# Performance work log

Hardware: AMD Instinct MI355X
Metric: run time of the kernel (lower is better)

Reference implementation:

```python
import jax, jax.numpy as jnp
import numpy as np

N = 100000
E = 3200000
IN_DIM = 512
HID = 256
NUM_CLASSES = 16
P_DROP = 0.5
EPS_BN = 1e-5


def setup_inputs() -> dict:
    key = jax.random.key(0)
    ks = jax.random.split(key, 6)
    x = jax.random.normal(ks[0], (N, IN_DIM), jnp.float32)
    edge_src = jax.random.randint(ks[1], (E,), 0, N, dtype=jnp.int32)
    edge_dst = jax.random.randint(ks[2], (E,), 0, N, dtype=jnp.int32)
    # Glorot-ish init for GraphConv weights (bias=False in the module)
    W1 = jax.random.normal(ks[3], (IN_DIM, HID), jnp.float32) / np.sqrt(IN_DIM).astype(np.float32)
    W2 = jax.random.normal(ks[4], (HID, NUM_CLASSES), jnp.float32) / np.sqrt(HID).astype(np.float32)
    W3 = jax.random.normal(ks[5], (HID, NUM_CLASSES), jnp.float32) / np.sqrt(HID).astype(np.float32)
    return {"x": x, "W1": W1, "W2": W2, "W3": W3,
            "edge_src": edge_src, "edge_dst": edge_dst}


def _graph_conv(h, W, edge_src, edge_dst, out_inv_sqrt, in_inv_sqrt):
    # DGL GraphConv, norm='both', bias=False:
    #   rst = D_in^{-1/2} * A_agg( D_out^{-1/2} * h @ W )
    # Apply W before aggregation (out_dim <= in_dim here); same math as DGL.
    h = h * out_inv_sqrt[:, None]          # [N, d_in]
    h = h @ W                              # [N, d_out]
    agg = jax.ops.segment_sum(h[edge_src], edge_dst, num_segments=h.shape[0])
    return agg * in_inv_sqrt[:, None]


def _dropout(key, x, p=P_DROP):
    keep = jax.random.bernoulli(key, 1.0 - p, x.shape)
    return jnp.where(keep, x / (1.0 - p), jnp.zeros((), x.dtype))


def reference(x, W1, W2, W3, edge_src, edge_dst):
    n = x.shape[0]
    ones = jnp.ones(edge_src.shape[0], x.dtype)
    out_deg = jax.ops.segment_sum(ones, edge_src, num_segments=n)
    in_deg = jax.ops.segment_sum(ones, edge_dst, num_segments=n)
    out_is = jnp.maximum(out_deg, 1.0) ** -0.5   # DGL clamps degree to min 1
    in_is = jnp.maximum(in_deg, 1.0) ** -0.5

    k1, k2a, k2b, keps = jax.random.split(jax.random.key(42), 4)

    # gc1 + relu
    h = _dropout(k1, x)
    h = jax.nn.relu(_graph_conv(h, W1, edge_src, edge_dst, out_is, in_is))

    # BatchNorm1d(affine=False, track_running_stats=False): batch stats
    mean = jnp.mean(h, axis=0)
    var = jnp.var(h, axis=0)
    h = (h - mean) * jax.lax.rsqrt(var + EPS_BN)

    # gc2 (mu) and gc3 (logvar), each with its own dropout of hidden1
    mu = _graph_conv(_dropout(k2a, h), W2, edge_src, edge_dst, out_is, in_is)
    logvar = _graph_conv(_dropout(k2b, h), W3, edge_src, edge_dst, out_is, in_is)

    # reparameterize (training): eps * exp(logvar) + mu  (note: exp(logvar), per source)
    eps = jax.random.normal(keps, mu.shape, mu.dtype)
    return eps * jnp.exp(logvar) + mu
```

## Files before the change

### kernel.cpp

```cpp
#include <hip/hip_runtime.h>
#include <stdint.h>

#define N_NODES 100000
#define N_EDGES 3200000
#define IN_DIM  512
#define HID     256
#define NCLS    16

#define DBLK   256
#define DCHUNK (N_EDGES / DBLK)
#define DWIN2  50000
#define NBKT   98
#define NTILE  ((N_NODES + 255) / 256)

typedef unsigned short u16;
typedef __attribute__((ext_vector_type(8))) short short8;
typedef __attribute__((ext_vector_type(4))) float float4v;

__device__ __forceinline__ float bf2f(u16 u) {
  return __uint_as_float(((uint32_t)u) << 16);
}
__device__ __forceinline__ u16 f2bf(float f) {
  uint32_t u = __float_as_uint(f);
  return (u16)((u + 0x7fffu + ((u >> 16) & 1u)) >> 16);
}
__device__ __forceinline__ void acc8(float* a, uint4 v) {
  a[0] += bf2f((u16)(v.x & 0xffffu)); a[1] += bf2f((u16)(v.x >> 16));
  a[2] += bf2f((u16)(v.y & 0xffffu)); a[3] += bf2f((u16)(v.y >> 16));
  a[4] += bf2f((u16)(v.z & 0xffffu)); a[5] += bf2f((u16)(v.z >> 16));
  a[6] += bf2f((u16)(v.w & 0xffffu)); a[7] += bf2f((u16)(v.w >> 16));
}

__device__ __forceinline__ void gload16(const void* g, void* l) {
  __builtin_amdgcn_global_load_lds(
      (const __attribute__((address_space(1))) uint32_t*)g,
      (__attribute__((address_space(3))) uint32_t*)l, 16, 0, 0);
}

__host__ __device__ __forceinline__ uint32_t rotl32(uint32_t v, int d) {
  return (v << d) | (v >> (32 - d));
}

__host__ __device__ __forceinline__ void threefry2x32(uint32_t k0, uint32_t k1,
    uint32_t x0, uint32_t x1, uint32_t& o0, uint32_t& o1) {
  uint32_t ks0 = k0, ks1 = k1, ks2 = k0 ^ k1 ^ 0x1BD11BDAu;
  x0 += ks0; x1 += ks1;
#define TF_R(r) { x0 += x1; x1 = rotl32(x1, r); x1 ^= x0; }
  TF_R(13) TF_R(15) TF_R(26) TF_R(6)
  x0 += ks1; x1 += ks2 + 1u;
  TF_R(17) TF_R(29) TF_R(16) TF_R(24)
  x0 += ks2; x1 += ks0 + 2u;
  TF_R(13) TF_R(15) TF_R(26) TF_R(6)
  x0 += ks0; x1 += ks1 + 3u;
  TF_R(17) TF_R(29) TF_R(16) TF_R(24)
  x0 += ks1; x1 += ks2 + 4u;
  TF_R(13) TF_R(15) TF_R(26) TF_R(6)
  x0 += ks2; x1 += ks0 + 5u;
#undef TF_R
  o0 = x0; o1 = x1;
}

__host__ __device__ __forceinline__ uint32_t tf_bits32(uint32_t k0, uint32_t k1, uint32_t idx) {
  uint32_t o0, o1;
  threefry2x32(k0, k1, 0u, idx, o0, o1);
  return o0 ^ o1;
}

__device__ __forceinline__ float erfinv_f32(float x) {
  float w = -log1pf(-x * x);
  float p;
  if (w < 5.0f) {
    w -= 2.5f;
    p = 2.81022636e-08f;
    p = fmaf(p, w, 3.43273939e-07f);
    p = fmaf(p, w, -3.5233877e-06f);
    p = fmaf(p, w, -4.39150654e-06f);
    p = fmaf(p, w, 0.00021858087f);
    p = fmaf(p, w, -0.00125372503f);
    p = fmaf(p, w, -0.00417768164f);
    p = fmaf(p, w, 0.246640727f);
    p = fmaf(p, w, 1.50140941f);
  } else {
    w = sqrtf(w) - 3.0f;
    p = -0.000200214257f;
    p = fmaf(p, w, 0.000100950558f);
    p = fmaf(p, w, 0.00134934322f);
    p = fmaf(p, w, -0.00367342844f);
    p = fmaf(p, w, 0.00573950773f);
    p = fmaf(p, w, -0.0076224613f);
    p = fmaf(p, w, 0.00943887047f);
    p = fmaf(p, w, 1.00167406f);
    p = fmaf(p, w, 2.83297682f);
  }
  return p * x;
}

__global__ __launch_bounds__(1024) void hist_k(
    const int* __restrict__ esrc, const int* __restrict__ edst,
    u16* __restrict__ P16, uint32_t* __restrict__ bofs_g) {
  __shared__ uint32_t h32[DWIN2 / 2];
  __shared__ uint32_t bcnt[NBKT + 1];
  const int b = blockIdx.x, tid = threadIdx.x;
  const int ebase = b * DCHUNK;
  if (tid < NBKT + 1) bcnt[tid] = 0u;
  for (int w = 0; w < 2; ++w) {
    const int lo = w * DWIN2;
    for (int i = tid; i < DWIN2 / 2; i += 1024) h32[i] = 0u;
    __syncthreads();
    for (int e = ebase + tid; e < ebase + DCHUNK; e += 1024) {
      int s = esrc[e], d = edst[e];
      unsigned su = (unsigned)(s - lo);
      if (su < (unsigned)DWIN2) atomicAdd(&h32[su >> 1], 1u << ((su & 1) * 16));
      unsigned du = (unsigned)(d - lo);
      if (du < (unsigned)DWIN2) atomicAdd(&h32[du >> 1], 0x100u << ((du & 1) * 16));
      if (w == 0) atomicAdd(&bcnt[d >> 10], 1u);
    }
    __syncthreads();
    for (int i = tid; i < DWIN2 / 2; i += 1024) {
      *(uint32_t*)(P16 + (size_t)b * N_NODES + lo + 2 * i) = h32[i];
    }
    __syncthreads();
  }
  if (tid == 0) {
    uint32_t run = 0;
    for (int k = 0; k < NBKT; ++k) { uint32_t c = bcnt[k]; bcnt[k] = run; run += c; }
    bcnt[NBKT] = run;
  }
  __syncthreads();
  if (tid < NBKT + 1) bofs_g[b * (NBKT + 1) + tid] = bcnt[tid];
}

__global__ void degsum_k(const u16* __restrict__ P16, float* __restrict__ out_is,
                         float* __restrict__ in_is, int* __restrict__ row_ofs,
                         int* __restrict__ tile_sum) {
  const int tid = threadIdx.x;
  const int n = blockIdx.x * 256 + tid;
  const int lane = tid & 63, wv = tid >> 6;
  uint32_t to = 0, ti = 0;
  if (n < N_NODES) {
#pragma unroll 8
    for (int b = 0; b < DBLK; ++b) {
      uint32_t v = P16[(size_t)b * N_NODES + n];
      to += v & 0xffu; ti += v >> 8;
    }
    out_is[n] = rsqrtf(fmaxf((float)to, 1.0f));
    in_is[n]  = rsqrtf(fmaxf((float)ti, 1.0f));
  }
  int sc = (int)ti;
#pragma unroll
  for (int d = 1; d < 64; d <<= 1) {
    int t = __shfl_up(sc, d, 64);
    if (lane >= d) sc += t;
  }
  __shared__ int ws[4];
  if (lane == 63) ws[wv] = sc;
  __syncthreads();
  int wbase = 0;
#pragma unroll
  for (int i = 0; i < 4; ++i) if (i < wv) wbase += ws[i];
  if (n < N_NODES) row_ofs[n] = wbase + sc - (int)ti;
  if (tid == 0) tile_sum[blockIdx.x] = ws[0] + ws[1] + ws[2] + ws[3];
}

__global__ void fixup_k(const int* __restrict__ tile_sum, int* __restrict__ row_ofs) {
  const int b = blockIdx.x, tid = threadIdx.x;
  const int lane = tid & 63, wv = tid >> 6;
  int v = 0;
  if (tid < b) v = tile_sum[tid];
  if (tid + 256 < b) v += tile_sum[tid + 256];
#pragma unroll
  for (int m = 1; m < 64; m <<= 1) v += __shfl_xor(v, m, 64);
  __shared__ int wr[4];
  if (lane == 0) wr[wv] = v;
  __syncthreads();
  const int base = wr[0] + wr[1] + wr[2] + wr[3];
  const int n = b * 256 + tid;
  if (n < N_NODES) row_ofs[n] += base;
  if (b == (int)gridDim.x - 1 && tid == 0) row_ofs[N_NODES] = base + tile_sum[b];
}

__global__ __launch_bounds__(1024) void partition_k(
    const int* __restrict__ esrc, const int* __restrict__ edst,
    const uint32_t* __restrict__ bofs_g, unsigned long long* __restrict__ ebuf) {
  __shared__ uint32_t bcur[NBKT];
  const int b = blockIdx.x, tid = threadIdx.x;
  if (tid < NBKT) bcur[tid] = bofs_g[b * (NBKT + 1) + tid];
  __syncthreads();
  const int ebase = b * DCHUNK;
  for (int e = ebase + tid; e < ebase + DCHUNK; e += 1024) {
    int d = edst[e], s = esrc[e];
    uint32_t slot = atomicAdd(&bcur[d >> 10], 1u);
    ebuf[(size_t)b * DCHUNK + slot] = ((unsigned long long)(uint32_t)s << 32) | (uint32_t)d;
  }
}

__global__ __launch_bounds__(1024) void bplace_k(
    const unsigned long long* __restrict__ ebuf, const uint32_t* __restrict__ bofs_g,
    const int* __restrict__ row_ofs, int* __restrict__ csr) {
  __shared__ uint32_t cur[1024];
  const int k = blockIdx.x, tid = threadIdx.x;
  const int lane = tid & 63, wv = tid >> 6;
  const int dbase = k << 10;
  int nd = N_NODES - dbase; if (nd > 1024) nd = 1024;
  if (tid < nd) cur[tid] = (uint32_t)row_ofs[dbase + tid];
  __syncthreads();
  for (int b = wv; b < DBLK; b += 16) {
    uint32_t st = bofs_g[b * (NBKT + 1) + k];
    uint32_t en = bofs_g[b * (NBKT + 1) + k + 1];
    for (uint32_t i = st + lane; i < en; i += 64) {
      unsigned long long v = ebuf[(size_t)b * DCHUNK + i];
      int d = (int)(uint32_t)(v & 0xffffffffu);
      int s = (int)(uint32_t)(v >> 32);
      uint32_t slot = atomicAdd(&cur[d - dbase], 1u);
      csr[slot] = s;
    }
  }
}

__global__ void cast_w_k(const float* __restrict__ W1, const float* __restrict__ W2,
                         const float* __restrict__ W3, u16* __restrict__ W1t,
                         u16* __restrict__ Wt23) {
  int idx = blockIdx.x * blockDim.x + threadIdx.x;
  if (idx < IN_DIM * HID) {
    int k = idx >> 8, n = idx & 255;
    W1t[n * IN_DIM + k] = f2bf(W1[idx]);
  } else {
    int t = idx - IN_DIM * HID;
    int n = t >> 8, k = t & 255;
    float v = (n < 16) ? W2[k * NCLS + n] : W3[k * NCLS + (n - 16)];
    Wt23[n * HID + k] = f2bf(v);
  }
}

#define G1_BM 128
#define G1_BKC 8
__global__ __launch_bounds__(512, 2) void gemm1_k(
    const float* __restrict__ x, const float* __restrict__ out_is,
    uint32_t k0, uint32_t k1,
    const u16* __restrict__ W1t, u16* __restrict__ X1b) {
  __shared__ u16 As[G1_BM * 64];
  __shared__ u16 Bs[256 * 64];
  const int tid = threadIdx.x;
  const int wid = tid >> 6, lane = tid & 63;
  const int wr = wid >> 2, wc = wid & 3;
  const int m16 = lane & 15, q = lane >> 4;
  const int srow = lane >> 3, schunk = lane & 7;
  const long base_row = (long)blockIdx.x * G1_BM;

  const int arow_l = tid >> 2, acp = tid & 3;
  const long agrow = base_row + arow_l;
  const long asrow = (agrow < N_NODES) ? agrow : (N_NODES - 1);
  const float asc = 2.0f * out_is[asrow];
  const float* xrow = x + asrow * IN_DIM;
  const int aw0 = ((2 * acp)     ^ (arow_l & 7)) * 8;
  const int aw1 = ((2 * acp + 1) ^ (arow_l & 7)) * 8;

  float4v acc[4][4];
#pragma unroll
  for (int i = 0; i < 4; ++i)
#pragma unroll
    for (int j = 0; j < 4; ++j) acc[i][j] = (float4v)0.0f;

  for (int ks = 0; ks < IN_DIM / 64; ++ks) {
    const int kbase = ks * 64 + acp * 16;
    float4 f0 = *(const float4*)(xrow + kbase);
    float4 f1 = *(const float4*)(xrow + kbase + 4);
    float4 f2 = *(const float4*)(xrow + kbase + 8);
    float4 f3 = *(const float4*)(xrow + kbase + 12);
    float xv[16] = {f0.x, f0.y, f0.z, f0.w, f1.x, f1.y, f1.z, f1.w,
                    f2.x, f2.y, f2.z, f2.w, f3.x, f3.y, f3.z, f3.w};
    const uint32_t ibase = (uint32_t)asrow * IN_DIM + (uint32_t)kbase;
    u16 ob[16];
#pragma unroll
    for (int j = 0; j < 16; ++j) {
      uint32_t bits = tf_bits32(k0, k1, ibase + (uint32_t)j);
      ob[j] = f2bf((bits >> 31) ? 0.0f : xv[j] * asc);
    }
    uint4 pka, pkb;
    pka.x = (uint32_t)ob[0] | ((uint32_t)ob[1] << 16);
    pka.y = (uint32_t)ob[2] | ((uint32_t)ob[3] << 16);
    pka.z = (uint32_t)ob[4] | ((uint32_t)ob[5] << 16);
    pka.w = (uint32_t)ob[6] | ((uint32_t)ob[7] << 16);
    pkb.x = (uint32_t)ob[8] | ((uint32_t)ob[9] << 16);
    pkb.y = (uint32_t)ob[10] | ((uint32_t)ob[11] << 16);
    pkb.z = (uint32_t)ob[12] | ((uint32_t)ob[13] << 16);
    pkb.w = (uint32_t)ob[14] | ((uint32_t)ob[15] << 16);
    *(uint4*)(As + arow_l * 64 + aw0) = pka;
    *(uint4*)(As + arow_l * 64 + aw1) = pkb;
#pragma unroll
    for (int i = 0; i < 4; ++i) {
      int j = wid * 4 + i;
      int n = j * 8 + srow;
      int gch = ks * G1_BKC + (schunk ^ (n & 7));
      gload16(W1t + (size_t)n * IN_DIM + gch * 8, Bs + j * 512);
    }
    __syncthreads();
#pragma unroll
    for (int kk = 0; kk < 2; ++kk) {
      short8 a[4], b[4];
      const int kq = kk * 4 + q;
      const int c = kq ^ (m16 & 7);
#pragma unroll
      for (int rt = 0; rt < 4; ++rt) {
        int row = wr * 64 + rt * 16 + m16;
        a[rt] = *(const short8*)(As + row * 64 + c * 8);
      }
#pragma unroll
      for (int ct = 0; ct < 4; ++ct) {
        int n = wc * 64 + ct * 16 + m16;
        b[ct] = *(const short8*)(Bs + n * 64 + c * 8);
      }
#pragma unroll
      for (int rt = 0; rt < 4; ++rt)
#pragma unroll
        for (int ct = 0; ct < 4; ++ct)
          acc[rt][ct] = __builtin_amdgcn_mfma_f32_16x16x32_bf16(a[rt], b[ct], acc[rt][ct], 0, 0, 0);
    }
    __syncthreads();
  }
#pragma unroll
  for (int rt = 0; rt < 4; ++rt) {
#pragma unroll
    for (int r = 0; r < 4; ++r) {
      long grow = base_row + wr * 64 + rt * 16 + q * 4 + r;
      if (grow < N_NODES) {
#pragma unroll
        for (int ct = 0; ct < 4; ++ct)
          X1b[grow * HID + wc * 64 + ct * 16 + m16] = f2bf(acc[rt][ct][r]);
      }
    }
  }
}

__global__ __launch_bounds__(256) void agg_relu_k(
    const u16* __restrict__ X1b, const int* __restrict__ row_ofs,
    const int* __restrict__ csr, const float* __restrict__ in_is,
    u16* __restrict__ h1b) {
  int d = blockIdx.x * 4 + (threadIdx.x >> 6);
  int lane = threadIdx.x & 63;
  int half = lane >> 5;
  int col = (lane & 31) * 8;
  int beg = row_ofs[d], end = row_ofs[d + 1];
  float a[8];
#pragma unroll
  for (int i = 0; i < 8; ++i) a[i] = 0.0f;
  int j = beg + half;
  for (; j + 14 < end; j += 16) {
    int s0 = csr[j],      s1 = csr[j + 2],  s2 = csr[j + 4],  s3 = csr[j + 6];
    int s4 = csr[j + 8],  s5 = csr[j + 10], s6 = csr[j + 12], s7 = csr[j + 14];
    uint4 v0 = *(const uint4*)(X1b + (size_t)s0 * HID + col);
    uint4 v1 = *(const uint4*)(X1b + (size_t)s1 * HID + col);
    uint4 v2 = *(const uint4*)(X1b + (size_t)s2 * HID + col);
    uint4 v3 = *(const uint4*)(X1b + (size_t)s3 * HID + col);
    uint4 v4 = *(const uint4*)(X1b + (size_t)s4 * HID + col);
    uint4 v5 = *(const uint4*)(X1b + (size_t)s5 * HID + col);
    uint4 v6 = *(const uint4*)(X1b + (size_t)s6 * HID + col);
    uint4 v7 = *(const uint4*)(X1b + (size_t)s7 * HID + col);
    acc8(a, v0); acc8(a, v1); acc8(a, v2); acc8(a, v3);
    acc8(a, v4); acc8(a, v5); acc8(a, v6); acc8(a, v7);
  }
  for (; j + 6 < end; j += 8) {
    int s0 = csr[j], s1 = csr[j + 2], s2 = csr[j + 4], s3 = csr[j + 6];
    uint4 v0 = *(const uint4*)(X1b + (size_t)s0 * HID + col);
    uint4 v1 = *(const uint4*)(X1b + (size_t)s1 * HID + col);
    uint4 v2 = *(const uint4*)(X1b + (size_t)s2 * HID + col);
    uint4 v3 = *(const uint4*)(X1b + (size_t)s3 * HID + col);
    acc8(a, v0); acc8(a, v1); acc8(a, v2); acc8(a, v3);
  }
  for (; j < end; j += 2) {
    uint4 v0 = *(const uint4*)(X1b + (size_t)csr[j] * HID + col);
    acc8(a, v0);
  }
#pragma unroll
  for (int i = 0; i < 8; ++i) a[i] += __shfl(a[i], lane ^ 32, 64);
  if (half == 0) {
    float is = in_is[d];
    u16 o[8];
#pragma unroll
    for (int i = 0; i < 8; ++i) o[i] = f2bf(fmaxf(a[i] * is, 0.0f));
    uint4 pk;
    pk.x = (uint32_t)o[0] | ((uint32_t)o[1] << 16);
    pk.y = (uint32_t)o[2] | ((uint32_t)o[3] << 16);
    pk.z = (uint32_t)o[4] | ((uint32_t)o[5] << 16);
    pk.w = (uint32_t)o[6] | ((uint32_t)o[7] << 16);
    *(uint4*)(h1b + (size_t)d * HID + col) = pk;
  }
}

__global__ __launch_bounds__(256) void bn_stats_k(const u16* __restrict__ h1b,
                                                  float* __restrict__ bn) {
  __shared__ float ls[512];
  const int tid = threadIdx.x;
  const int cb = (tid & 31) * 8;
  const int ms = tid >> 5;
  float s[8], s2[8];
#pragma unroll
  for (int i = 0; i < 8; ++i) { s[i] = 0.f; s2[i] = 0.f; }
  for (int m = ms;; m += 8) {
    int r = blockIdx.x + 256 * m;
    if (r >= N_NODES) break;
    uint4 v = *(const uint4*)(h1b + (size_t)r * HID + cb);
    float f[8];
    f[0] = bf2f((u16)(v.x & 0xffffu)); f[1] = bf2f((u16)(v.x >> 16));
    f[2] = bf2f((u16)(v.y & 0xffffu)); f[3] = bf2f((u16)(v.y >> 16));
    f[4] = bf2f((u16)(v.z & 0xffffu)); f[5] = bf2f((u16)(v.z >> 16));
    f[6] = bf2f((u16)(v.w & 0xffffu)); f[7] = bf2f((u16)(v.w >> 16));
#pragma unroll
    for (int i = 0; i < 8; ++i) { s[i] += f[i]; s2[i] += f[i] * f[i]; }
  }
  ls[tid] = 0.f; ls[tid + 256] = 0.f;
  __syncthreads();
#pragma unroll
  for (int i = 0; i < 8; ++i) {
    atomicAdd(&ls[cb + i], s[i]);
    atomicAdd(&ls[256 + cb + i], s2[i]);
  }
  __syncthreads();
  atomicAdd(&bn[tid], ls[tid]);
  atomicAdd(&bn[HID + tid], ls[256 + tid]);
}

#define WLS 264
__global__ __launch_bounds__(256) void gemm23_k(
    const u16* __restrict__ h1b, const u16* __restrict__ Wt23,
    uint32_t ka0, uint32_t ka1, uint32_t kb0, uint32_t kb1,
    const float* __restrict__ out_is, const float* __restrict__ bn,
    u16* __restrict__ XMLV) {
  __shared__ u16 Wls[32 * WLS];
  __shared__ float cB[HID], cA[HID];
  const int tid = threadIdx.x;
#pragma unroll
  for (int i = 0; i < 4; ++i) {
    int idx = tid + i * 256;
    int n = idx >> 5, c = idx & 31;
    *(uint4*)(Wls + n * WLS + c * 8) = ((const uint4*)Wt23)[idx];
  }
  {
    float mean = bn[tid] * (1.0f / (float)N_NODES);
    float var = bn[HID + tid] * (1.0f / (float)N_NODES) - mean * mean;
    float istd = rsqrtf(var + 1e-5f);
    cB[tid] = istd;
    cA[tid] = -mean * istd;
  }
  __syncthreads();

  const int wv = tid >> 6, lane = tid & 63;
  const int m = lane & 15, q = lane >> 4;
  const long arow = (long)blockIdx.x * 64 + wv * 16 + m;
  const bool valid = arow < N_NODES;
  const float osc = valid ? 2.0f * out_is[arow] : 0.0f;
  const uint32_t rbase = (uint32_t)(valid ? arow : 0) * HID;

  float4v accM = (float4v)0.0f, accL = (float4v)0.0f;
  for (int kc = 0; kc < HID; kc += 32) {
    const int kof = kc + q * 8;
    uint4 hv = make_uint4(0, 0, 0, 0);
    if (valid) hv = *(const uint4*)(h1b + arow * HID + kof);
    float4 B0 = *(const float4*)(cB + kof);
    float4 B1 = *(const float4*)(cB + kof + 4);
    float4 A0 = *(const float4*)(cA + kof);
    float4 A1 = *(const float4*)(cA + kof + 4);
    float hval[8] = {
      bf2f((u16)(hv.x & 0xffffu)), bf2f((u16)(hv.x >> 16)),
      bf2f((u16)(hv.y & 0xffffu)), bf2f((u16)(hv.y >> 16)),
      bf2f((u16)(hv.z & 0xffffu)), bf2f((u16)(hv.z >> 16)),
      bf2f((u16)(hv.w & 0xffffu)), bf2f((u16)(hv.w >> 16))};
    float nb[8] = {B0.x, B0.y, B0.z, B0.w, B1.x, B1.y, B1.z, B1.w};
    float na[8] = {A0.x, A0.y, A0.z, A0.w, A1.x, A1.y, A1.z, A1.w};
    const uint32_t ibase = rbase + (uint32_t)kof;
    short8 Aa, Ab;
#pragma unroll
    for (int jj = 0; jj < 8; ++jj) {
      float t = fmaf(hval[jj], nb[jj], na[jj]) * osc;
      u16 tb = f2bf(t);
      uint32_t ba = tf_bits32(ka0, ka1, ibase + (uint32_t)jj);
      uint32_t bb = tf_bits32(kb0, kb1, ibase + (uint32_t)jj);
      Aa[jj] = (short)((ba >> 31) ? 0 : tb);
      Ab[jj] = (short)((bb >> 31) ? 0 : tb);
    }
    short8 Bm = *(const short8*)(Wls + m * WLS + kof);
    short8 Bl = *(const short8*)(Wls + (16 + m) * WLS + kof);
    accM = __builtin_amdgcn_mfma_f32_16x16x32_bf16(Aa, Bm, accM, 0, 0, 0);
    accL = __builtin_amdgcn_mfma_f32_16x16x32_bf16(Ab, Bl, accL, 0, 0, 0);
  }
#pragma unroll
  for (int r = 0; r < 4; ++r) {
    long srow = (long)blockIdx.x * 64 + wv * 16 + q * 4 + r;
    if (srow < N_NODES) {
      XMLV[srow * 32 + m]      = f2bf(accM[r]);
      XMLV[srow * 32 + 16 + m] = f2bf(accL[r]);
    }
  }
}

__global__ __launch_bounds__(256) void agg_final_k(
    const u16* __restrict__ XMLV, const int* __restrict__ row_ofs,
    const int* __restrict__ csr, const float* __restrict__ in_is,
    uint32_t ke0, uint32_t ke1, float* __restrict__ out) {
  int g = blockIdx.x * 4 + (threadIdx.x >> 6);
  int lane = threadIdx.x & 63;
  int half = lane >> 5, c = lane & 31;
  int beg = row_ofs[g], end = row_ofs[g + 1];
  float s = 0.f;
  int j = beg + half;
  for (; j + 14 < end; j += 16) {
    int s0 = csr[j],      s1 = csr[j + 2],  s2 = csr[j + 4],  s3 = csr[j + 6];
    int s4 = csr[j + 8],  s5 = csr[j + 10], s6 = csr[j + 12], s7 = csr[j + 14];
    float v0 = bf2f(XMLV[(size_t)s0 * 32 + c]);
    float v1 = bf2f(XMLV[(size_t)s1 * 32 + c]);
    float v2 = bf2f(XMLV[(size_t)s2 * 32 + c]);
    float v3 = bf2f(XMLV[(size_t)s3 * 32 + c]);
    float v4 = bf2f(XMLV[(size_t)s4 * 32 + c]);
    float v5 = bf2f(XMLV[(size_t)s5 * 32 + c]);
    float v6 = bf2f(XMLV[(size_t)s6 * 32 + c]);
    float v7 = bf2f(XMLV[(size_t)s7 * 32 + c]);
    s += v0; s += v1; s += v2; s += v3;
    s += v4; s += v5; s += v6; s += v7;
  }
#pragma unroll
  for (int k = 0; k < 8; ++k) {
    int e = j + 2 * k;
    if (e < end) s += bf2f(XMLV[(size_t)csr[e] * 32 + c]);
  }
  s += __shfl(s, lane ^ 32, 64);
  if (half == 0) {
    s *= in_is[g];
    float other = __shfl(s, lane ^ 16, 64);
    if (c < 16) {
      uint32_t i = (uint32_t)(g * NCLS + c);
      uint32_t bits = tf_bits32(ke0, ke1, i);
      float f = __uint_as_float((bits >> 9) | 0x3f800000u) - 1.0f;
      const float lo = -0.99999994f;
      float u = fmaxf(lo, fmaf(f, 2.0f, lo));
      float eps = 1.41421356f * erfinv_f32(u);
      out[i] = eps * expf(other) + s;
    }
  }
}

extern "C" void kernel_launch(void* const* d_in, const int* in_sizes, int n_in,
                              void* d_out, int out_size, void* d_ws, size_t ws_size,
                              hipStream_t stream) {
  (void)in_sizes; (void)n_in; (void)out_size; (void)ws_size;
  const float* x  = (const float*)d_in[0];
  const float* W1 = (const float*)d_in[1];
  const float* W2 = (const float*)d_in[2];
  const float* W3 = (const float*)d_in[3];
  const int* esrc = (const int*)d_in[4];
  const int* edst = (const int*)d_in[5];
  float* out = (float*)d_out;

  uint32_t kb[8];
  for (int j = 0; j < 4; ++j)
    threefry2x32(0u, 42u, 0u, (uint32_t)j, kb[2 * j], kb[2 * j + 1]);

  char* p = (char*)d_ws;
  auto take = [&](size_t bytes) -> void* {
    void* r = (void*)p;
    p += (bytes + 255) & ~(size_t)255;
    return r;
  };
  u16* P16       = (u16*)take(sizeof(u16) * (size_t)DBLK * N_NODES);
  unsigned long long* ebuf = (unsigned long long*)take(sizeof(unsigned long long) * (size_t)N_EDGES);
  u16* X1b       = (u16*)take(sizeof(u16) * (size_t)N_NODES * HID);
  u16* h1b       = (u16*)take(sizeof(u16) * (size_t)N_NODES * HID);
  u16* XMLV      = (u16*)take(sizeof(u16) * (size_t)N_NODES * 32);
  u16* W1t       = (u16*)take(sizeof(u16) * (size_t)IN_DIM * HID);
  u16* Wt23      = (u16*)take(sizeof(u16) * 32 * HID);
  uint32_t* bofs_g = (uint32_t*)take(sizeof(uint32_t) * (size_t)DBLK * (NBKT + 1));
  int* tile_sum  = (int*)take(sizeof(int) * NTILE);
  float* out_is  = (float*)take(sizeof(float) * N_NODES);
  float* in_is   = (float*)take(sizeof(float) * N_NODES);
  int* row_ofs   = (int*)take(sizeof(int) * (N_NODES + 1));
  int* csr       = (int*)take(sizeof(int) * N_EDGES);
  float* bn      = (float*)take(sizeof(float) * 1024);

  hipMemsetAsync(bn, 0, sizeof(float) * 512, stream);

  hist_k<<<DBLK, 1024, 0, stream>>>(esrc, edst, P16, bofs_g);
  degsum_k<<<NTILE, 256, 0, stream>>>(P16, out_is, in_is, row_ofs, tile_sum);
  fixup_k<<<NTILE, 256, 0, stream>>>(tile_sum, row_ofs);
  partition_k<<<DBLK, 1024, 0, stream>>>(esrc, edst, bofs_g, ebuf);
  bplace_k<<<NBKT, 1024, 0, stream>>>(ebuf, bofs_g, row_ofs, csr);

  cast_w_k<<<(IN_DIM * HID + 32 * HID) / 256, 256, 0, stream>>>(W1, W2, W3, W1t, Wt23);

  gemm1_k<<<(N_NODES + G1_BM - 1) / G1_BM, 512, 0, stream>>>(x, out_is, kb[0], kb[1], W1t, X1b);
  agg_relu_k<<<N_NODES / 4, 256, 0, stream>>>(X1b, row_ofs, csr, in_is, h1b);
  bn_stats_k<<<256, 256, 0, stream>>>(h1b, bn);
  gemm23_k<<<(N_NODES + 63) / 64, 256, 0, stream>>>(h1b, Wt23, kb[2], kb[3], kb[4], kb[5],
                                                    out_is, bn, XMLV);
  agg_final_k<<<N_NODES / 4, 256, 0, stream>>>(XMLV, row_ofs, csr, in_is, kb[6], kb[7], out);
}
```

Measured before the change: 912.8 us.

## Replace per-block degree histograms with global atomics and fuse partition pass

Degree counting no longer builds 256 per-block 16-bit shared-memory histograms that are written out and then reduced column by column. Each edge now does global atomic increments on one degree array, and the bucket partition pass is folded into the same kernel, so one launch and the large P16 traffic go away. The cost is 6.4M global atomics spread over 100k addresses, plus an extra memset. Edge reads stay at two passes over the edge arrays, both inside one kernel.

Measured after the change: 1.116 ms. 22.3% more time.

```diff
diff --git a/kernel.cpp b/kernel.cpp
--- a/kernel.cpp
+++ b/kernel.cpp
@@ -9,7 +9,6 @@
 
 #define DBLK   256
 #define DCHUNK (N_EDGES / DBLK)
-#define DWIN2  50000
 #define NBKT   98
 #define NTILE  ((N_NODES + 255) / 256)
 
@@ -95,32 +94,22 @@
   return p * x;
 }
 
-__global__ __launch_bounds__(1024) void hist_k(
+__global__ __launch_bounds__(1024) void prep1_k(
     const int* __restrict__ esrc, const int* __restrict__ edst,
-    u16* __restrict__ P16, uint32_t* __restrict__ bofs_g) {
-  __shared__ uint32_t h32[DWIN2 / 2];
+    uint32_t* __restrict__ deg, uint32_t* __restrict__ bofs_g,
+    unsigned long long* __restrict__ ebuf) {
   __shared__ uint32_t bcnt[NBKT + 1];
   const int b = blockIdx.x, tid = threadIdx.x;
+  if (tid < NBKT + 1) bcnt[tid] = 0u;
+  __syncthreads();
   const int ebase = b * DCHUNK;
-  if (tid < NBKT + 1) bcnt[tid] = 0u;
-  for (int w = 0; w < 2; ++w) {
-    const int lo = w * DWIN2;
-    for (int i = tid; i < DWIN2 / 2; i += 1024) h32[i] = 0u;
-    __syncthreads();
-    for (int e = ebase + tid; e < ebase + DCHUNK; e += 1024) {
-      int s = esrc[e], d = edst[e];
-      unsigned su = (unsigned)(s - lo);
-      if (su < (unsigned)DWIN2) atomicAdd(&h32[su >> 1], 1u << ((su & 1) * 16));
-      unsigned du = (unsigned)(d - lo);
-      if (du < (unsigned)DWIN2) atomicAdd(&h32[du >> 1], 0x100u << ((du & 1) * 16));
-      if (w == 0) atomicAdd(&bcnt[d >> 10], 1u);
-    }
-    __syncthreads();
-    for (int i = tid; i < DWIN2 / 2; i += 1024) {
-      *(uint32_t*)(P16 + (size_t)b * N_NODES + lo + 2 * i) = h32[i];
-    }
-    __syncthreads();
-  }
+  for (int e = ebase + tid; e < ebase + DCHUNK; e += 1024) {
+    int s = esrc[e], d = edst[e];
+    atomicAdd(&deg[s], 1u);
+    atomicAdd(&deg[N_NODES + d], 1u);
+    atomicAdd(&bcnt[d >> 10], 1u);
+  }
+  __syncthreads();
   if (tid == 0) {
     uint32_t run = 0;
     for (int k = 0; k < NBKT; ++k) { uint32_t c = bcnt[k]; bcnt[k] = run; run += c; }
@@ -128,21 +117,24 @@
   }
   __syncthreads();
   if (tid < NBKT + 1) bofs_g[b * (NBKT + 1) + tid] = bcnt[tid];
-}
-
-__global__ void degsum_k(const u16* __restrict__ P16, float* __restrict__ out_is,
-                         float* __restrict__ in_is, int* __restrict__ row_ofs,
-                         int* __restrict__ tile_sum) {
+  __syncthreads();
+  for (int e = ebase + tid; e < ebase + DCHUNK; e += 1024) {
+    int d = edst[e], s = esrc[e];
+    uint32_t slot = atomicAdd(&bcnt[d >> 10], 1u);
+    ebuf[(size_t)b * DCHUNK + slot] = ((unsigned long long)(uint32_t)s << 32) | (uint32_t)d;
+  }
+}
+
+__global__ void scan1_k(const uint32_t* __restrict__ deg, float* __restrict__ out_is,
+                        float* __restrict__ in_is, int* __restrict__ row_ofs,
+                        int* __restrict__ tile_sum) {
   const int tid = threadIdx.x;
   const int n = blockIdx.x * 256 + tid;
   const int lane = tid & 63, wv = tid >> 6;
-  uint32_t to = 0, ti = 0;
+  uint32_t ti = 0;
   if (n < N_NODES) {
-#pragma unroll 8
-    for (int b = 0; b < DBLK; ++b) {
-      uint32_t v = P16[(size_t)b * N_NODES + n];
-      to += v & 0xffu; ti += v >> 8;
-    }
+    uint32_t to = deg[n];
+    ti = deg[N_NODES + n];
     out_is[n] = rsqrtf(fmaxf((float)to, 1.0f));
     in_is[n]  = rsqrtf(fmaxf((float)ti, 1.0f));
   }
@@ -177,21 +169,6 @@
   const int n = b * 256 + tid;
   if (n < N_NODES) row_ofs[n] += base;
   if (b == (int)gridDim.x - 1 && tid == 0) row_ofs[N_NODES] = base + tile_sum[b];
-}
-
-__global__ __launch_bounds__(1024) void partition_k(
-    const int* __restrict__ esrc, const int* __restrict__ edst,
-    const uint32_t* __restrict__ bofs_g, unsigned long long* __restrict__ ebuf) {
-  __shared__ uint32_t bcur[NBKT];
-  const int b = blockIdx.x, tid = threadIdx.x;
-  if (tid < NBKT) bcur[tid] = bofs_g[b * (NBKT + 1) + tid];
-  __syncthreads();
-  const int ebase = b * DCHUNK;
-  for (int e = ebase + tid; e < ebase + DCHUNK; e += 1024) {
-    int d = edst[e], s = esrc[e];
-    uint32_t slot = atomicAdd(&bcur[d >> 10], 1u);
-    ebuf[(size_t)b * DCHUNK + slot] = ((unsigned long long)(uint32_t)s << 32) | (uint32_t)d;
-  }
 }
 
 __global__ __launch_bounds__(1024) void bplace_k(
@@ -560,13 +537,13 @@
     p += (bytes + 255) & ~(size_t)255;
     return r;
   };
-  u16* P16       = (u16*)take(sizeof(u16) * (size_t)DBLK * N_NODES);
   unsigned long long* ebuf = (unsigned long long*)take(sizeof(unsigned long long) * (size_t)N_EDGES);
   u16* X1b       = (u16*)take(sizeof(u16) * (size_t)N_NODES * HID);
   u16* h1b       = (u16*)take(sizeof(u16) * (size_t)N_NODES * HID);
   u16* XMLV      = (u16*)take(sizeof(u16) * (size_t)N_NODES * 32);
   u16* W1t       = (u16*)take(sizeof(u16) * (size_t)IN_DIM * HID);
   u16* Wt23      = (u16*)take(sizeof(u16) * 32 * HID);
+  uint32_t* deg  = (uint32_t*)take(sizeof(uint32_t) * 2 * N_NODES);
   uint32_t* bofs_g = (uint32_t*)take(sizeof(uint32_t) * (size_t)DBLK * (NBKT + 1));
   int* tile_sum  = (int*)take(sizeof(int) * NTILE);
   float* out_is  = (float*)take(sizeof(float) * N_NODES);
@@ -576,11 +553,11 @@
   float* bn      = (float*)take(sizeof(float) * 1024);
 
   hipMemsetAsync(bn, 0, sizeof(float) * 512, stream);
-
-  hist_k<<<DBLK, 1024, 0, stream>>>(esrc, edst, P16, bofs_g);
-  degsum_k<<<NTILE, 256, 0, stream>>>(P16, out_is, in_is, row_ofs, tile_sum);
+  hipMemsetAsync(deg, 0, sizeof(uint32_t) * 2 * N_NODES, stream);
+
+  prep1_k<<<DBLK, 1024, 0, stream>>>(esrc, edst, deg, bofs_g, ebuf);
+  scan1_k<<<NTILE, 256, 0, stream>>>(deg, out_is, in_is, row_ofs, tile_sum);
   fixup_k<<<NTILE, 256, 0, stream>>>(tile_sum, row_ofs);
-  partition_k<<<DBLK, 1024, 0, stream>>>(esrc, edst, bofs_g, ebuf);
   bplace_k<<<NBKT, 1024, 0, stream>>>(ebuf, bofs_g, row_ofs, csr);
 
   cast_w_k<<<(IN_DIM * HID + 32 * HID) / 256, 256, 0, stream>>>(W1, W2, W3, W1t, Wt23);
```
